# Optimization experiments

Hardware: AMD Instinct MI355X
Metric: run time of the kernel (lower is better)

## Reference

```python
import jax, jax.numpy as jnp
import numpy as np

B, H, S, D = 4, 16, 2048, 64

def setup_inputs() -> dict:
    key = jax.random.key(0)
    kq, kk, kv, km = jax.random.split(key, 4)
    q = jax.random.normal(kq, (B, H, S, D), dtype=jnp.float32)
    k = jax.random.normal(kk, (B, H, S, D), dtype=jnp.float32)
    v = jax.random.normal(kv, (B, H, S, D), dtype=jnp.float32)
    mask = jax.random.randint(km, (B, H, S, S), 0, 2, dtype=jnp.int32)
    return {"q": q, "k": k, "v": v, "mask": mask}

def reference(q, k, v, mask):
    d_k = q.shape[-1]
    scale = 1.0 / jnp.sqrt(jnp.asarray(d_k, dtype=q.dtype))
    # scores: [B, H, Sq, Sk]
    scores = jnp.einsum('bhqd,bhkd->bhqk', q, k) * scale
    scores = jnp.where(mask == 0, jnp.asarray(-10000.0, dtype=scores.dtype), scores)
    attn = jax.nn.softmax(scores, axis=-1)
    out = jnp.einsum('bhqk,bhkd->bhqd', attn, v)
    return (out, attn)
```

## Files before the change

kernel.cpp:

```cpp
#include <hip/hip_runtime.h>
#include <hip/hip_bf16.h>

typedef short bf16x8 __attribute__((ext_vector_type(8)));
typedef float f32x4 __attribute__((ext_vector_type(4)));
typedef unsigned short u16x8 __attribute__((ext_vector_type(8)));

#define DEVI static __device__ __forceinline__

constexpr int Bb = 4, Hh = 16, Ss = 2048, Dd = 64;
constexpr int BH = Bb * Hh;
constexpr float SCALE = 0.125f;
constexpr long QKV_ELEMS = (long)BH * Ss * Dd;

DEVI unsigned short f2bf(float f) {
  __hip_bfloat16 h = __float2bfloat16(f);
  unsigned short u;
  __builtin_memcpy(&u, &h, 2);
  return u;
}
DEVI float bflo(unsigned int u) { unsigned int x = u << 16;        float f; __builtin_memcpy(&f, &x, 4); return f; }
DEVI float bfhi(unsigned int u) { unsigned int x = u & 0xffff0000u; float f; __builtin_memcpy(&f, &x, 4); return f; }

DEVI int pidx(int q, int k) { return (q << 12) + ((k << 1) ^ ((q & 7) << 4)); }

DEVI bf16x8 cvt8(const float* p) {
  float4 a = *reinterpret_cast<const float4*>(p);
  float4 b = *reinterpret_cast<const float4*>(p + 4);
  bf16x8 r;
  r[0] = (short)f2bf(a.x); r[1] = (short)f2bf(a.y); r[2] = (short)f2bf(a.z); r[3] = (short)f2bf(a.w);
  r[4] = (short)f2bf(b.x); r[5] = (short)f2bf(b.y); r[6] = (short)f2bf(b.z); r[7] = (short)f2bf(b.w);
  return r;
}

__global__ __launch_bounds__(256) void cvt_qk(const float* __restrict__ q, const float* __restrict__ k,
                                              unsigned short* __restrict__ qb, unsigned short* __restrict__ kb)
{
  const long i = ((long)blockIdx.x * 256 + threadIdx.x) * 4;
  if (i >= QKV_ELEMS) return;
  const float4 a = *reinterpret_cast<const float4*>(q + i);
  ushort4 oa; oa.x = f2bf(a.x); oa.y = f2bf(a.y); oa.z = f2bf(a.z); oa.w = f2bf(a.w);
  *reinterpret_cast<ushort4*>(qb + i) = oa;
  const float4 b = *reinterpret_cast<const float4*>(k + i);
  ushort4 ob; ob.x = f2bf(b.x); ob.y = f2bf(b.y); ob.z = f2bf(b.z); ob.w = f2bf(b.w);
  *reinterpret_cast<ushort4*>(kb + i) = ob;
}

__global__ __launch_bounds__(256) void cvt_vt(const float* __restrict__ v, unsigned short* __restrict__ vt)
{
  __shared__ float tile[64][65];
  const int bh = blockIdx.x >> 5;
  const int s0 = (blockIdx.x & 31) << 6;
  const int t  = threadIdx.x;
  {
    const int c = (t & 15) << 2;
    const float* src = v + ((long)bh * Ss + s0) * Dd;
    for (int rr = (t >> 4); rr < 64; rr += 16) {
      const float4 a = *reinterpret_cast<const float4*>(src + rr * Dd + c);
      tile[rr][c] = a.x; tile[rr][c + 1] = a.y; tile[rr][c + 2] = a.z; tile[rr][c + 3] = a.w;
    }
  }
  __syncthreads();
  {
    const int d  = t >> 2;
    const int sc = (t & 3) << 4;
    unsigned short* dst = vt + ((long)bh * Dd + d) * Ss + s0 + sc;
    u16x8 v0, v1;
#pragma unroll
    for (int j = 0; j < 8; ++j) v0[j] = f2bf(tile[sc + j][d]);
#pragma unroll
    for (int j = 0; j < 8; ++j) v1[j] = f2bf(tile[sc + 8 + j][d]);
    *reinterpret_cast<u16x8*>(dst)     = v0;
    *reinterpret_cast<u16x8*>(dst + 8) = v1;
  }
}

template<bool PRE>
__global__ __launch_bounds__(256, 2)
void attn_main(const float* __restrict__ qf, const float* __restrict__ kf,
               const float* __restrict__ vf, const int* __restrict__ mask,
               const unsigned short* __restrict__ qb,
               const unsigned short* __restrict__ kbp,
               const unsigned short* __restrict__ vt,
               float* __restrict__ out, float* __restrict__ attn)
{
  __shared__ __align__(16) char Pb[16 * 2048 * 2];
  __shared__ float rpart[4][16];
  __shared__ float rinv[16];

  const int tid  = threadIdx.x;
  const int wave = tid >> 6;
  const int lane = tid & 63;
  const int l15  = lane & 15;
  const int lg   = lane >> 4;

  const int bh    = blockIdx.x >> 7;
  const int qbase = (blockIdx.x & 127) << 4;

  bf16x8 qfrag0, qfrag1;
  {
    const long qrow = (long)(bh * Ss + qbase + l15) * Dd + lg * 8;
    if (PRE) {
      qfrag0 = *reinterpret_cast<const bf16x8*>(qb + qrow);
      qfrag1 = *reinterpret_cast<const bf16x8*>(qb + qrow + 32);
    } else {
      qfrag0 = cvt8(qf + qrow);
      qfrag1 = cvt8(qf + qrow + 32);
    }
  }

  float psum = 0.f;
  const long mrow = (long)(bh * Ss + qbase + l15) * Ss;

  for (int kt = 0; kt < Ss; kt += 64) {
    const int key0 = kt + (wave << 4);
    bf16x8 kfrag0, kfrag1;
    const long krow = (long)(bh * Ss + key0 + l15) * Dd + lg * 8;
    if (PRE) {
      kfrag0 = *reinterpret_cast<const bf16x8*>(kbp + krow);
      kfrag1 = *reinterpret_cast<const bf16x8*>(kbp + krow + 32);
    } else {
      kfrag0 = cvt8(kf + krow);
      kfrag1 = cvt8(kf + krow + 32);
    }
    const int k0 = key0 + (lg << 2);
    const int4 m4 = *reinterpret_cast<const int4*>(mask + mrow + k0);
    f32x4 acc = {0.f, 0.f, 0.f, 0.f};
    acc = __builtin_amdgcn_mfma_f32_16x16x32_bf16(kfrag0, qfrag0, acc, 0, 0, 0);
    acc = __builtin_amdgcn_mfma_f32_16x16x32_bf16(kfrag1, qfrag1, acc, 0, 0, 0);
    const float p0 = m4.x ? __expf(acc[0] * SCALE) : 0.f;
    const float p1 = m4.y ? __expf(acc[1] * SCALE) : 0.f;
    const float p2 = m4.z ? __expf(acc[2] * SCALE) : 0.f;
    const float p3 = m4.w ? __expf(acc[3] * SCALE) : 0.f;
    psum += (p0 + p1) + (p2 + p3);
    uint2 w2;
    w2.x = (unsigned)f2bf(p0) | ((unsigned)f2bf(p1) << 16);
    w2.y = (unsigned)f2bf(p2) | ((unsigned)f2bf(p3) << 16);
    *reinterpret_cast<uint2*>(Pb + pidx(l15, k0)) = w2;
  }

  psum += __shfl_xor(psum, 16);
  psum += __shfl_xor(psum, 32);
  if (lane < 16) rpart[wave][l15] = psum;
  __syncthreads();
  if (tid < 16) {
    const float t = rpart[0][tid] + rpart[1][tid] + rpart[2][tid] + rpart[3][tid];
    rinv[tid] = (t > 0.f) ? (1.f / t) : 0.f;
  }
  __syncthreads();

  {
    const int r  = tid >> 4;
    const int cs = (tid & 15) << 3;
    const float inv = rinv[r];
    float* arow = attn + (long)(bh * Ss + qbase + r) * Ss;
#pragma unroll
    for (int it = 0; it < 16; ++it) {
      const int c0 = cs + (it << 7);
      const uint4 pk = *reinterpret_cast<const uint4*>(Pb + pidx(r, c0));
      float4 o0, o1;
      o0.x = bflo(pk.x) * inv; o0.y = bfhi(pk.x) * inv;
      o0.z = bflo(pk.y) * inv; o0.w = bfhi(pk.y) * inv;
      o1.x = bflo(pk.z) * inv; o1.y = bfhi(pk.z) * inv;
      o1.z = bflo(pk.w) * inv; o1.w = bfhi(pk.w) * inv;
      *reinterpret_cast<float4*>(arow + c0)     = o0;
      *reinterpret_cast<float4*>(arow + c0 + 4) = o1;
    }
  }

  {
    const int dcol = (wave << 4) + l15;
    f32x4 oacc = {0.f, 0.f, 0.f, 0.f};
    const unsigned short* vrow = PRE ? (vt + (long)(bh * Dd + dcol) * Ss) : nullptr;
    const float* vcolf = PRE ? nullptr : (vf + (long)bh * Ss * Dd + dcol);
    for (int kk = 0; kk < Ss; kk += 32) {
      const int ka = kk + (lg << 3);
      const bf16x8 afrag = *reinterpret_cast<const bf16x8*>(Pb + pidx(l15, ka));
      bf16x8 bfrag;
      if (PRE) {
        bfrag = *reinterpret_cast<const bf16x8*>(vrow + ka);
      } else {
#pragma unroll
        for (int e = 0; e < 8; ++e) bfrag[e] = (short)f2bf(vcolf[(long)(ka + e) * Dd]);
      }
      oacc = __builtin_amdgcn_mfma_f32_16x16x32_bf16(afrag, bfrag, oacc, 0, 0, 0);
    }
    float* obase = out + (long)(bh * Ss + qbase) * Dd + dcol;
#pragma unroll
    for (int rg = 0; rg < 4; ++rg) {
      const int qrow = (lg << 2) + rg;
      obase[qrow * Dd] = oacc[rg] * rinv[qrow];
    }
  }
}

extern "C" void kernel_launch(void* const* d_in, const int* in_sizes, int n_in,
                              void* d_out, int out_size, void* d_ws, size_t ws_size,
                              hipStream_t stream)
{
  const float* q    = (const float*)d_in[0];
  const float* k    = (const float*)d_in[1];
  const float* v    = (const float*)d_in[2];
  const int*   mask = (const int*)d_in[3];
  float* out  = (float*)d_out;
  float* attn = out + QKV_ELEMS;

  const size_t need = (size_t)QKV_ELEMS * 2 * 3;
  if (ws_size >= need) {
    unsigned short* qb = (unsigned short*)d_ws;
    unsigned short* kb = qb + QKV_ELEMS;
    unsigned short* vt = kb + QKV_ELEMS;
    hipLaunchKernelGGL(cvt_qk, dim3((unsigned)(QKV_ELEMS / 1024)), dim3(256), 0, stream, q, k, qb, kb);
    hipLaunchKernelGGL(cvt_vt, dim3(BH * 32), dim3(256), 0, stream, v, vt);
    hipLaunchKernelGGL((attn_main<true>), dim3(BH * 128), dim3(256), 0, stream,
                       q, k, v, mask, qb, kb, vt, out, attn);
  } else {
    hipLaunchKernelGGL((attn_main<false>), dim3(BH * 128), dim3(256), 0, stream,
                       q, k, v, mask, nullptr, nullptr, nullptr, out, attn);
  }
}
```

Measured before the change: 813.2 us.

## Pre-pack int32 mask into bitmask and use nontemporal output stores

Adds a separate kernel that reads the int32 mask with fully coalesced nontemporal loads and packs it into a 64-bit ballot bitmask in the workspace. The main attention kernel then reads 4 mask bits per lane instead of an int4 per lane. The attn and out stores become nontemporal to avoid polluting cache with write-once data. Mask bytes from HBM are still read once overall, so the gain depends on better access patterns. The cost is an extra launch and a larger workspace requirement, which could push execution onto the slow fallback path if the workspace is too small.

```diff
diff --git a/kernel.cpp b/kernel.cpp
--- a/kernel.cpp
+++ b/kernel.cpp
@@ -11,6 +11,7 @@
 constexpr int BH = Bb * Hh;
 constexpr float SCALE = 0.125f;
 constexpr long QKV_ELEMS = (long)BH * Ss * Dd;
+constexpr long MASK_ELEMS = (long)BH * Ss * Ss;
 
 DEVI unsigned short f2bf(float f) {
   __hip_bfloat16 h = __float2bfloat16(f);
@@ -30,6 +31,25 @@
   r[0] = (short)f2bf(a.x); r[1] = (short)f2bf(a.y); r[2] = (short)f2bf(a.z); r[3] = (short)f2bf(a.w);
   r[4] = (short)f2bf(b.x); r[5] = (short)f2bf(b.y); r[6] = (short)f2bf(b.z); r[7] = (short)f2bf(b.w);
   return r;
+}
+
+__global__ __launch_bounds__(256) void bitpack(const int* __restrict__ mask,
+                                               unsigned long long* __restrict__ bits)
+{
+  const long wid = (((long)blockIdx.x * 256 + threadIdx.x) >> 6);
+  const int lane = threadIdx.x & 63;
+  const long NW = ((long)gridDim.x * 256) >> 6;
+  for (long W = wid; W < (MASK_ELEMS >> 8); W += NW) {
+    const int* p = mask + (W << 8) + lane;
+    const unsigned long long b0 = __ballot(__builtin_nontemporal_load(p) != 0);
+    const unsigned long long b1 = __ballot(__builtin_nontemporal_load(p + 64) != 0);
+    const unsigned long long b2 = __ballot(__builtin_nontemporal_load(p + 128) != 0);
+    const unsigned long long b3 = __ballot(__builtin_nontemporal_load(p + 192) != 0);
+    if (lane == 0) {
+      ulonglong4 o; o.x = b0; o.y = b1; o.z = b2; o.w = b3;
+      *reinterpret_cast<ulonglong4*>(bits + (W << 2)) = o;
+    }
+  }
 }
 
 __global__ __launch_bounds__(256) void cvt_qk(const float* __restrict__ q, const float* __restrict__ k,
@@ -81,6 +101,7 @@
                const unsigned short* __restrict__ qb,
                const unsigned short* __restrict__ kbp,
                const unsigned short* __restrict__ vt,
+               const unsigned long long* __restrict__ bits,
                float* __restrict__ out, float* __restrict__ attn)
 {
   __shared__ __align__(16) char Pb[16 * 2048 * 2];
@@ -123,14 +144,22 @@
       kfrag1 = cvt8(kf + krow + 32);
     }
     const int k0 = key0 + (lg << 2);
-    const int4 m4 = *reinterpret_cast<const int4*>(mask + mrow + k0);
+    unsigned mm;
+    if (PRE) {
+      const unsigned long long e = (unsigned long long)(mrow + k0);
+      const unsigned long long w = bits[e >> 6];
+      mm = (unsigned)(w >> ((int)e & 63)) & 0xFu;
+    } else {
+      const int4 m4 = *reinterpret_cast<const int4*>(mask + mrow + k0);
+      mm = (m4.x ? 1u : 0u) | (m4.y ? 2u : 0u) | (m4.z ? 4u : 0u) | (m4.w ? 8u : 0u);
+    }
     f32x4 acc = {0.f, 0.f, 0.f, 0.f};
     acc = __builtin_amdgcn_mfma_f32_16x16x32_bf16(kfrag0, qfrag0, acc, 0, 0, 0);
     acc = __builtin_amdgcn_mfma_f32_16x16x32_bf16(kfrag1, qfrag1, acc, 0, 0, 0);
-    const float p0 = m4.x ? __expf(acc[0] * SCALE) : 0.f;
-    const float p1 = m4.y ? __expf(acc[1] * SCALE) : 0.f;
-    const float p2 = m4.z ? __expf(acc[2] * SCALE) : 0.f;
-    const float p3 = m4.w ? __expf(acc[3] * SCALE) : 0.f;
+    const float p0 = (mm & 1u) ? __expf(acc[0] * SCALE) : 0.f;
+    const float p1 = (mm & 2u) ? __expf(acc[1] * SCALE) : 0.f;
+    const float p2 = (mm & 4u) ? __expf(acc[2] * SCALE) : 0.f;
+    const float p3 = (mm & 8u) ? __expf(acc[3] * SCALE) : 0.f;
     psum += (p0 + p1) + (p2 + p3);
     uint2 w2;
     w2.x = (unsigned)f2bf(p0) | ((unsigned)f2bf(p1) << 16);
@@ -157,13 +186,13 @@
     for (int it = 0; it < 16; ++it) {
       const int c0 = cs + (it << 7);
       const uint4 pk = *reinterpret_cast<const uint4*>(Pb + pidx(r, c0));
-      float4 o0, o1;
-      o0.x = bflo(pk.x) * inv; o0.y = bfhi(pk.x) * inv;
-      o0.z = bflo(pk.y) * inv; o0.w = bfhi(pk.y) * inv;
-      o1.x = bflo(pk.z) * inv; o1.y = bfhi(pk.z) * inv;
-      o1.z = bflo(pk.w) * inv; o1.w = bfhi(pk.w) * inv;
-      *reinterpret_cast<float4*>(arow + c0)     = o0;
-      *reinterpret_cast<float4*>(arow + c0 + 4) = o1;
+      f32x4 o0, o1;
+      o0[0] = bflo(pk.x) * inv; o0[1] = bfhi(pk.x) * inv;
+      o0[2] = bflo(pk.y) * inv; o0[3] = bfhi(pk.y) * inv;
+      o1[0] = bflo(pk.z) * inv; o1[1] = bfhi(pk.z) * inv;
+      o1[2] = bflo(pk.w) * inv; o1[3] = bfhi(pk.w) * inv;
+      __builtin_nontemporal_store(o0, reinterpret_cast<f32x4*>(arow + c0));
+      __builtin_nontemporal_store(o1, reinterpret_cast<f32x4*>(arow + c0 + 4));
     }
   }
 
@@ -188,7 +217,7 @@
 #pragma unroll
     for (int rg = 0; rg < 4; ++rg) {
       const int qrow = (lg << 2) + rg;
-      obase[qrow * Dd] = oacc[rg] * rinv[qrow];
+      __builtin_nontemporal_store(oacc[rg] * rinv[qrow], obase + qrow * Dd);
     }
   }
 }
@@ -204,17 +233,21 @@
   float* out  = (float*)d_out;
   float* attn = out + QKV_ELEMS;
 
-  const size_t need = (size_t)QKV_ELEMS * 2 * 3;
+  const size_t bf16_bytes = (size_t)QKV_ELEMS * 2 * 3;
+  const size_t bits_bytes = (size_t)(MASK_ELEMS >> 3);
+  const size_t need = bf16_bytes + bits_bytes;
   if (ws_size >= need) {
     unsigned short* qb = (unsigned short*)d_ws;
     unsigned short* kb = qb + QKV_ELEMS;
     unsigned short* vt = kb + QKV_ELEMS;
+    unsigned long long* bits = (unsigned long long*)((char*)d_ws + bf16_bytes);
+    hipLaunchKernelGGL(bitpack, dim3(2048), dim3(256), 0, stream, mask, bits);
     hipLaunchKernelGGL(cvt_qk, dim3((unsigned)(QKV_ELEMS / 1024)), dim3(256), 0, stream, q, k, qb, kb);
     hipLaunchKernelGGL(cvt_vt, dim3(BH * 32), dim3(256), 0, stream, v, vt);
     hipLaunchKernelGGL((attn_main<true>), dim3(BH * 128), dim3(256), 0, stream,
-                       q, k, v, mask, qb, kb, vt, out, attn);
+                       q, k, v, mask, qb, kb, vt, bits, out, attn);
   } else {
     hipLaunchKernelGGL((attn_main<false>), dim3(BH * 128), dim3(256), 0, stream,
-                       q, k, v, mask, nullptr, nullptr, nullptr, out, attn);
-  }
-}
+                       q, k, v, mask, nullptr, nullptr, nullptr, nullptr, out, attn);
+  }
+}
```

Measured after the change: 945.8 us. 1.16x slower.
